# Kernel optimization log

Measured on AMD Instinct MI355X. Metric: run time of the kernel, lower is better.

The kernel has to match this reference:

```python
import jax, jax.numpy as jnp
import numpy as np

N_HEAD = 8
EPS_LN = 1e-5
EPS_SM = 1e-16


def _mlp(x, w1, b1, g, beta, w2, b2):
    # Linear -> ReLU -> LayerNorm -> Linear (matches nn.Sequential in torch module)
    h = jax.nn.relu(x @ w1 + b1)
    mu = jnp.mean(h, axis=-1, keepdims=True)
    var = jnp.mean((h - mu) ** 2, axis=-1, keepdims=True)
    h = (h - mu) * jax.lax.rsqrt(var + EPS_LN) * g + beta
    return h @ w2 + b2


def setup_inputs() -> dict:
    B, L, D, E, Fe, H = 4, 4096, 128, 262144, 5, N_HEAD
    ks = jax.random.split(jax.random.key(0), 20)
    s = 0.02
    p = lambda i, sh: jax.random.normal(ks[i], sh, jnp.float32) * s
    z = lambda n: jnp.zeros((n,), jnp.float32)
    inp = {
        "key": jax.random.normal(ks[0], (B, L, D), jnp.float32),
        "value": jax.random.normal(ks[1], (B, L, D), jnp.float32),
        "query": jax.random.normal(ks[2], (B, L, D), jnp.float32),
        "edge_feats": jax.random.normal(ks[3], (E, Fe), jnp.float32),
        "atten_masks": jnp.zeros((E,), jnp.float32),  # present in signature, unused in forward
        "batch_indices": jax.random.randint(ks[4], (E,), 0, B),
        "head_indices": jax.random.randint(ks[5], (E,), 0, L),
        "tail_indices": jax.random.randint(ks[6], (E,), 0, L),
        "key_w": p(7, (D, D)), "key_b": z(D),
        "query_w": p(8, (D, D)), "query_b": z(D),
        "value_w": p(9, (D, D)), "value_b": z(D),
        "proj_w": p(10, (D, D)), "proj_b": z(D),
        "ea_w1": p(11, (Fe, D)), "ea_b1": z(D), "ea_g": jnp.ones((D,), jnp.float32), "ea_beta": z(D), "ea_w2": p(12, (D, H)), "ea_b2": z(H),
        "ek_w1": p(13, (Fe, D)), "ek_b1": z(D), "ek_g": jnp.ones((D,), jnp.float32), "ek_beta": z(D), "ek_w2": p(14, (D, D)), "ek_b2": z(D),
        "ev_w1": p(15, (Fe, D)), "ev_b1": z(D), "ev_g": jnp.ones((D,), jnp.float32), "ev_beta": z(D), "ev_w2": p(16, (D, D)), "ev_b2": z(D),
    }
    return inp


def reference(key, value, query, edge_feats, atten_masks,
              batch_indices, head_indices, tail_indices,
              key_w, key_b, query_w, query_b, value_w, value_b, proj_w, proj_b,
              ea_w1, ea_b1, ea_g, ea_beta, ea_w2, ea_b2,
              ek_w1, ek_b1, ek_g, ek_beta, ek_w2, ek_b2,
              ev_w1, ev_b1, ev_g, ev_beta, ev_w2, ev_b2):
    B, L, D = query.shape
    H = N_HEAD
    dh = D // H
    N = B * L
    # node projections -> [B*L, H, dh]
    k = (key @ key_w + key_b).reshape(N, H, dh)
    q = (query @ query_w + query_b).reshape(N, H, dh)
    v = (value @ value_w + value_b).reshape(N, H, dh)
    heads = batch_indices * L + head_indices  # destination node per edge
    tails = batch_indices * L + tail_indices  # source node per edge
    # per-edge gather + edge-conditioned k/v
    qs = q[heads]
    ks = k[tails] + _mlp(edge_feats, ek_w1, ek_b1, ek_g, ek_beta, ek_w2, ek_b2).reshape(-1, H, dh)
    vs = v[tails] + _mlp(edge_feats, ev_w1, ev_b1, ev_g, ev_beta, ev_w2, ev_b2).reshape(-1, H, dh)
    w = jnp.sum(ks * qs, axis=-1) + _mlp(edge_feats, ea_w1, ea_b1, ea_g, ea_beta, ea_w2, ea_b2)  # [E, H]
    # segment softmax over edges grouped by destination node
    m = jax.ops.segment_max(w, heads, num_segments=N)
    ex = jnp.exp(w - m[heads])
    denom = jax.ops.segment_sum(ex, heads, num_segments=N)
    att = ex / (denom[heads] + EPS_SM)  # [E, H]
    # weighted scatter-sum combine
    y = jax.ops.segment_sum(att[:, :, None] * vs, heads, num_segments=N).reshape(B, L, D)
    return y @ proj_w + proj_b
```

## Files before the change

### kernel.cpp

```cpp
#include <hip/hip_runtime.h>
#include <hip/hip_bf16.h>

#define D      128
#define NHEAD  8
#define FE     5
#define LSEQ   4096
#define EPB    64
#define NNODE  16384
#define EPS_LN 1e-5f
#define EPS_SM 1e-16f

typedef unsigned short ushort_t;
typedef __bf16 bf16x8 __attribute__((ext_vector_type(8)));
typedef float  f32x4  __attribute__((ext_vector_type(4)));

__device__ __forceinline__ ushort_t f2bf(float x) {
    __hip_bfloat16 b = __float2bfloat16(x);
    return __builtin_bit_cast(unsigned short, b);
}
__device__ __forceinline__ float bf2f(ushort_t u) {
    __hip_bfloat16 b = __builtin_bit_cast(__hip_bfloat16, u);
    return __bfloat162float(b);
}

union Pk8 { ushort_t u[8]; uint4 v; };

__global__ __launch_bounds__(256) void setup_kernel(
    const float* __restrict__ key, const float* __restrict__ value,
    const float* __restrict__ query,
    const float* __restrict__ key_w, const float* __restrict__ key_b,
    const float* __restrict__ value_w, const float* __restrict__ value_b,
    const float* __restrict__ query_w, const float* __restrict__ query_b,
    ushort_t* __restrict__ k16, ushort_t* __restrict__ v16, ushort_t* __restrict__ q16,
    const float* __restrict__ ekw2, const float* __restrict__ evw2,
    const float* __restrict__ eaw2,
    ushort_t* __restrict__ eksw, ushort_t* __restrict__ evsw, ushort_t* __restrict__ easw,
    const int* __restrict__ bidx, const int* __restrict__ hidx,
    int* __restrict__ cnt, int nqb, int E)
{
    __shared__ float xs[2][D][20];
    const int t  = threadIdx.x;
    const int nq = 3 * nqb;

    if ((int)blockIdx.x < nq) {
        const int which = blockIdx.x / nqb;
        const int r0    = (blockIdx.x % nqb) * 32;
        const float* X = (which == 0) ? key   : (which == 1) ? value   : query;
        const float* W = (which == 0) ? key_w : (which == 1) ? value_w : query_w;
        const float* bias = (which == 0) ? key_b : (which == 1) ? value_b : query_b;
        ushort_t* Y = (which == 0) ? k16 : (which == 1) ? v16 : q16;

        const int rg = t >> 7, j = t & 127;
        const int rbase = r0 + rg * 16;
        {
            float tmp[16];
            #pragma unroll
            for (int r = 0; r < 16; ++r) tmp[r] = X[(size_t)(rbase + r) * D + j];
            #pragma unroll
            for (int c = 0; c < 4; ++c)
                *(float4*)&xs[rg][j][c * 4] = float4{tmp[c*4], tmp[c*4+1], tmp[c*4+2], tmp[c*4+3]};
        }
        __syncthreads();
        float acc[16];
        const float b = bias[j];
        #pragma unroll
        for (int r = 0; r < 16; ++r) acc[r] = b;
        #pragma unroll 4
        for (int i = 0; i < D; ++i) {
            const float w = W[i * D + j];
            #pragma unroll
            for (int c = 0; c < 4; ++c) {
                const float4 x4 = *(const float4*)&xs[rg][i][c * 4];
                acc[c*4+0] = fmaf(x4.x, w, acc[c*4+0]);
                acc[c*4+1] = fmaf(x4.y, w, acc[c*4+1]);
                acc[c*4+2] = fmaf(x4.z, w, acc[c*4+2]);
                acc[c*4+3] = fmaf(x4.w, w, acc[c*4+3]);
            }
        }
        #pragma unroll
        for (int r = 0; r < 16; ++r) Y[(size_t)(rbase + r) * D + j] = f2bf(acc[r]);
        return;
    }

    const int b2 = blockIdx.x - nq;
    if (b2 < 17) {
        const int g = b2 * 256 + t;
        const float* src; ushort_t* dst; int frag, ncols, nvalid;
        if (g < 2048)      { src = ekw2; dst = eksw; frag = g;        ncols = 128; nvalid = 128; }
        else if (g < 4096) { src = evw2; dst = evsw; frag = g - 2048; ncols = 128; nvalid = 128; }
        else if (g < 4352) { src = eaw2; dst = easw; frag = g - 4096; ncols = 8;   nvalid = 8; }
        else return;
        const int s = (frag >> 6) & 3;
        const int l = frag & 63;
        const int n = ((frag >> 8) << 4) + (l & 15);
        Pk8 pk;
        #pragma unroll
        for (int j = 0; j < 8; ++j) {
            const int k = s * 32 + (l >> 4) * 8 + j;
            const float v = (n < nvalid) ? src[k * ncols + n] : 0.f;
            pk.u[j] = f2bf(v);
        }
        *(uint4*)(dst + (size_t)frag * 8) = pk.v;
        return;
    }

    const int e = (b2 - 17) * 256 + t;
    if (e < E) atomicAdd(&cnt[bidx[e] * LSEQ + hidx[e]], 1);
}

__global__ __launch_bounds__(1024) void scan16k(
    const int* __restrict__ cnt, int* __restrict__ base)
{
    __shared__ int part[1024];
    const int t = threadIdx.x;
    int v[16], ex[16], s = 0;
    #pragma unroll
    for (int i = 0; i < 16; ++i) v[i] = cnt[t * 16 + i];
    #pragma unroll
    for (int i = 0; i < 16; ++i) { ex[i] = s; s += v[i]; }
    part[t] = s;
    __syncthreads();
    for (int off = 1; off < 1024; off <<= 1) {
        const int x = (t >= off) ? part[t - off] : 0;
        __syncthreads();
        part[t] += x;
        __syncthreads();
    }
    const int boff = (t > 0) ? part[t - 1] : 0;
    #pragma unroll
    for (int i = 0; i < 16; ++i) base[t * 16 + i] = boff + ex[i];
    if (t == 1023) base[NNODE] = boff + s;
}

__global__ __launch_bounds__(128) void out_gemm(
    const float* __restrict__ num, const float* __restrict__ W,
    const float* __restrict__ bias, float* __restrict__ Y)
{
    __shared__ float xs[D][20];
    const int j  = threadIdx.x;
    const int r0 = blockIdx.x * 16;
    {
        float tmp[16];
        #pragma unroll
        for (int r = 0; r < 16; ++r) tmp[r] = num[(size_t)(r0 + r) * D + j];
        #pragma unroll
        for (int c = 0; c < 4; ++c)
            *(float4*)&xs[j][c * 4] = float4{tmp[c*4], tmp[c*4+1], tmp[c*4+2], tmp[c*4+3]};
    }
    __syncthreads();
    float acc[16];
    const float b = bias[j];
    #pragma unroll
    for (int r = 0; r < 16; ++r) acc[r] = b;
    #pragma unroll 4
    for (int i = 0; i < D; ++i) {
        const float w = W[i * D + j];
        #pragma unroll
        for (int c = 0; c < 4; ++c) {
            const float4 x4 = *(const float4*)&xs[i][c * 4];
            acc[c*4+0] = fmaf(x4.x, w, acc[c*4+0]);
            acc[c*4+1] = fmaf(x4.y, w, acc[c*4+1]);
            acc[c*4+2] = fmaf(x4.z, w, acc[c*4+2]);
            acc[c*4+3] = fmaf(x4.w, w, acc[c*4+3]);
        }
    }
    #pragma unroll
    for (int r = 0; r < 16; ++r) Y[(size_t)(r0 + r) * D + j] = acc[r];
}

__global__ __launch_bounds__(256, 4) void edge_kernel(
    const float* __restrict__ edge_feats,
    const int* __restrict__ bidx, const int* __restrict__ hidx, const int* __restrict__ tidx,
    const float* __restrict__ ea_w1, const float* __restrict__ ea_b1,
    const float* __restrict__ ea_g,  const float* __restrict__ ea_be, const float* __restrict__ ea_b2,
    const float* __restrict__ ek_w1, const float* __restrict__ ek_b1,
    const float* __restrict__ ek_g,  const float* __restrict__ ek_be, const float* __restrict__ ek_b2,
    const float* __restrict__ ev_w1, const float* __restrict__ ev_b1,
    const float* __restrict__ ev_g,  const float* __restrict__ ev_be, const float* __restrict__ ev_b2,
    const ushort_t* __restrict__ easw, const ushort_t* __restrict__ eksw, const ushort_t* __restrict__ evsw,
    const ushort_t* __restrict__ k16, const ushort_t* __restrict__ q16, const ushort_t* __restrict__ v16,
    const int* __restrict__ base, int* __restrict__ cnt, int* __restrict__ order,
    float* __restrict__ ex_ws, ushort_t* __restrict__ vs_ws)
{
    __shared__ float pw1[3][FE * D];
    __shared__ float pb1[3][D], pg[3][D], pbe[3][D];
    __shared__ float pb2k[D], pb2v[D], pb2a[NHEAD];
    __shared__ float ef_s[EPB][FE];
    __shared__ int   eh_s[EPB], et_s[EPB];

    const int t   = threadIdx.x;
    const int e0g = blockIdx.x * EPB;

    for (int i = t; i < FE * D; i += 256) { pw1[0][i] = ea_w1[i]; pw1[1][i] = ek_w1[i]; pw1[2][i] = ev_w1[i]; }
    if (t < D) {
        pb1[0][t] = ea_b1[t]; pb1[1][t] = ek_b1[t]; pb1[2][t] = ev_b1[t];
        pg [0][t] = ea_g [t]; pg [1][t] = ek_g [t]; pg [2][t] = ev_g [t];
        pbe[0][t] = ea_be[t]; pbe[1][t] = ek_be[t]; pbe[2][t] = ev_be[t];
        pb2k[t] = ek_b2[t];   pb2v[t] = ev_b2[t];
        if (t < NHEAD) pb2a[t] = ea_b2[t];
    }
    for (int i = t; i < EPB * FE; i += 256) ((float*)ef_s)[i] = edge_feats[(size_t)e0g * FE + i];
    if (t < EPB) {
        const int bb = bidx[e0g + t];
        const int nh = bb * LSEQ + hidx[e0g + t];
        eh_s[t] = nh;
        et_s[t] = bb * LSEQ + tidx[e0g + t];
        const int slot = atomicSub(&cnt[nh], 1) - 1;
        order[base[nh] + slot] = e0g + t;
    }
    __syncthreads();

    const int mt   = t >> 6;
    const int l    = t & 63;
    const int qt   = l & 3;
    const int per  = l >> 2;
    const int row0 = (l >> 4) * 4;
    const int colb = l & 15;
    const int src  = 4 * colb + (l >> 4);
    const int bsrc = (l & 48);

    int tn[4], hnn[4];
    #pragma unroll
    for (int r = 0; r < 4; ++r) { tn[r] = et_s[mt*16 + row0 + r]; hnn[r] = eh_s[mt*16 + row0 + r]; }

    float efr[FE];
    #pragma unroll
    for (int f = 0; f < FE; ++f) efr[f] = ef_s[mt*16 + per][f];

    auto first_layer = [&](int m, uint4 pk[4]) {
        const float4* w1v = (const float4*)&pw1[m][0];
        const float4* b1v = (const float4*)&pb1[m][0];
        const float4* gv  = (const float4*)&pg[m][0];
        const float4* bev = (const float4*)&pbe[m][0];
        float4 hv[4][2];
        float s1 = 0.f, s2 = 0.f;
        #pragma unroll
        for (int s = 0; s < 4; ++s) {
            #pragma unroll
            for (int hc = 0; hc < 2; ++hc) {
                const int idx = s * 8 + qt * 2 + hc;
                float4 a = b1v[idx];
                #pragma unroll
                for (int f = 0; f < FE; ++f) {
                    const float sc = efr[f];
                    const float4 w = w1v[f * 32 + idx];
                    a.x = fmaf(sc, w.x, a.x); a.y = fmaf(sc, w.y, a.y);
                    a.z = fmaf(sc, w.z, a.z); a.w = fmaf(sc, w.w, a.w);
                }
                a.x = fmaxf(a.x, 0.f); a.y = fmaxf(a.y, 0.f);
                a.z = fmaxf(a.z, 0.f); a.w = fmaxf(a.w, 0.f);
                hv[s][hc] = a;
                s1 += a.x + a.y + a.z + a.w;
                s2 += a.x*a.x + a.y*a.y + a.z*a.z + a.w*a.w;
            }
        }
        s1 += __shfl_xor(s1, 1); s1 += __shfl_xor(s1, 2);
        s2 += __shfl_xor(s2, 1); s2 += __shfl_xor(s2, 2);
        const float mu = s1 * (1.f / 128.f);
        const float rs = rsqrtf(s2 * (1.f / 128.f) - mu * mu + EPS_LN);
        #pragma unroll
        for (int s = 0; s < 4; ++s) {
            const int idx = s * 8 + qt * 2;
            const float4 x0 = hv[s][0], x1 = hv[s][1];
            const float4 g0 = gv[idx], g1 = gv[idx + 1];
            const float4 b0 = bev[idx], b1 = bev[idx + 1];
            Pk8 p8;
            p8.u[0] = f2bf(fmaf((x0.x - mu) * rs, g0.x, b0.x));
            p8.u[1] = f2bf(fmaf((x0.y - mu) * rs, g0.y, b0.y));
            p8.u[2] = f2bf(fmaf((x0.z - mu) * rs, g0.z, b0.z));
            p8.u[3] = f2bf(fmaf((x0.w - mu) * rs, g0.w, b0.w));
            p8.u[4] = f2bf(fmaf((x1.x - mu) * rs, g1.x, b1.x));
            p8.u[5] = f2bf(fmaf((x1.y - mu) * rs, g1.y, b1.y));
            p8.u[6] = f2bf(fmaf((x1.z - mu) * rs, g1.z, b1.z));
            p8.u[7] = f2bf(fmaf((x1.w - mu) * rs, g1.w, b1.w));
            pk[s] = p8.v;
        }
    };

    auto gather_afr = [&](const uint4 pk[4], bf16x8 afr[4]) {
        #pragma unroll
        for (int s = 0; s < 4; ++s) {
            uint4 w;
            w.x = (unsigned)__shfl((int)pk[s].x, src);
            w.y = (unsigned)__shfl((int)pk[s].y, src);
            w.z = (unsigned)__shfl((int)pk[s].z, src);
            w.w = (unsigned)__shfl((int)pk[s].w, src);
            afr[s] = __builtin_bit_cast(bf16x8, w);
        }
    };

    uint4 pk[4];
    bf16x8 afr[4];

    float eaacc[4];
    first_layer(0, pk);
    gather_afr(pk, afr);
    {
        f32x4 acc = {0.f, 0.f, 0.f, 0.f};
        #pragma unroll
        for (int s = 0; s < 4; ++s) {
            const bf16x8 bfr = *(const bf16x8*)(easw + (size_t)(s * 64 + l) * 8);
            acc = __builtin_amdgcn_mfma_f32_16x16x32_bf16(afr[s], bfr, acc, 0, 0, 0);
        }
        #pragma unroll
        for (int r = 0; r < 4; ++r) eaacc[r] = acc[r];
    }

    first_layer(1, pk);
    gather_afr(pk, afr);
    #pragma unroll
    for (int nt = 0; nt < NHEAD; ++nt) {
        f32x4 acc = {0.f, 0.f, 0.f, 0.f};
        #pragma unroll
        for (int s = 0; s < 4; ++s) {
            const bf16x8 bfr = *(const bf16x8*)(eksw + (size_t)((nt * 4 + s) * 64 + l) * 8);
            acc = __builtin_amdgcn_mfma_f32_16x16x32_bf16(afr[s], bfr, acc, 0, 0, 0);
        }
        const int col = nt * 16 + colb;
        const float b2 = pb2k[col];
        const float ba = pb2a[nt];
        float pr[4];
        #pragma unroll
        for (int r = 0; r < 4; ++r)
            pr[r] = (acc[r] + b2 + bf2f(k16[(size_t)tn[r] * D + col]))
                    * bf2f(q16[(size_t)hnn[r] * D + col]);
        #pragma unroll
        for (int m = 1; m < 16; m <<= 1) {
            #pragma unroll
            for (int r = 0; r < 4; ++r) pr[r] += __shfl_xor(pr[r], m);
        }
        #pragma unroll
        for (int r = 0; r < 4; ++r) {
            const float ea = __shfl(eaacc[r], bsrc | nt);
            const float ex = __expf(pr[r] + ea + ba);
            if (colb == nt)
                ex_ws[(size_t)(e0g + mt*16 + row0 + r) * NHEAD + nt] = ex;
        }
    }

    first_layer(2, pk);
    gather_afr(pk, afr);
    #pragma unroll
    for (int nt = 0; nt < NHEAD; ++nt) {
        f32x4 acc = {0.f, 0.f, 0.f, 0.f};
        #pragma unroll
        for (int s = 0; s < 4; ++s) {
            const bf16x8 bfr = *(const bf16x8*)(evsw + (size_t)((nt * 4 + s) * 64 + l) * 8);
            acc = __builtin_amdgcn_mfma_f32_16x16x32_bf16(afr[s], bfr, acc, 0, 0, 0);
        }
        const int col = nt * 16 + colb;
        const float b2 = pb2v[col];
        #pragma unroll
        for (int r = 0; r < 4; ++r) {
            const float vs = acc[r] + b2 + bf2f(v16[(size_t)tn[r] * D + col]);
            vs_ws[(size_t)(e0g + mt*16 + row0 + r) * D + col] = f2bf(vs);
        }
    }
}

__global__ __launch_bounds__(128) void agg_kernel(
    const int* __restrict__ order, const int* __restrict__ base,
    const float* __restrict__ ex_ws, const ushort_t* __restrict__ vs_ws,
    float* __restrict__ y_ws)
{
    const int n  = blockIdx.x;
    const int j  = threadIdx.x;
    const int h  = j >> 4;
    const int s0 = base[n], s1 = base[n + 1];

    float acc = 0.f, den = 0.f;
    int i = s0;
    for (; i + 8 <= s1; i += 8) {
        int e[8];
        #pragma unroll
        for (int r = 0; r < 8; ++r) e[r] = order[i + r];
        float exv[8], vsv[8];
        #pragma unroll
        for (int r = 0; r < 8; ++r) {
            exv[r] = ex_ws[(size_t)e[r] * NHEAD + h];
            vsv[r] = bf2f(vs_ws[(size_t)e[r] * D + j]);
        }
        #pragma unroll
        for (int r = 0; r < 8; ++r) {
            den += exv[r];
            acc = fmaf(exv[r], vsv[r], acc);
        }
    }
    for (; i < s1; ++i) {
        const int e = order[i];
        const float ex = ex_ws[(size_t)e * NHEAD + h];
        den += ex;
        acc = fmaf(ex, bf2f(vs_ws[(size_t)e * D + j]), acc);
    }
    y_ws[(size_t)n * D + j] = acc / (den + EPS_SM);
}

extern "C" void kernel_launch(void* const* d_in, const int* in_sizes, int n_in,
                              void* d_out, int out_size, void* d_ws, size_t ws_size,
                              hipStream_t stream)
{
    const float* key        = (const float*)d_in[0];
    const float* value      = (const float*)d_in[1];
    const float* query      = (const float*)d_in[2];
    const float* edge_feats = (const float*)d_in[3];
    const int*   bidx       = (const int*)d_in[5];
    const int*   hidx       = (const int*)d_in[6];
    const int*   tidx       = (const int*)d_in[7];
    const float* key_w   = (const float*)d_in[8];  const float* key_b   = (const float*)d_in[9];
    const float* query_w = (const float*)d_in[10]; const float* query_b = (const float*)d_in[11];
    const float* value_w = (const float*)d_in[12]; const float* value_b = (const float*)d_in[13];
    const float* proj_w  = (const float*)d_in[14]; const float* proj_b  = (const float*)d_in[15];

    const int N = in_sizes[0] / D;
    const int E = in_sizes[5];

    char* ws = (char*)d_ws;
    ushort_t* k16   = (ushort_t*)ws; ws += (size_t)N * D * 2;
    ushort_t* q16   = (ushort_t*)ws; ws += (size_t)N * D * 2;
    ushort_t* v16   = (ushort_t*)ws; ws += (size_t)N * D * 2;
    float* y_ws     = (float*)ws;    ws += (size_t)N * D * 4;
    float* ex_ws    = (float*)ws;    ws += (size_t)E * NHEAD * 4;
    ushort_t* vs_ws = (ushort_t*)ws; ws += (size_t)E * D * 2;
    ushort_t* eksw  = (ushort_t*)ws; ws += (size_t)2048 * 8 * 2;
    ushort_t* evsw  = (ushort_t*)ws; ws += (size_t)2048 * 8 * 2;
    ushort_t* easw  = (ushort_t*)ws; ws += (size_t)256 * 8 * 2;
    int* order = (int*)ws;  ws += (size_t)E * 4;
    int* base  = (int*)ws;  ws += (size_t)(N + 1) * 4;
    int* cnt   = (int*)ws;  ws += (size_t)N * 4;

    const int nqb = N / 32;
    const int nhist = (E + 255) / 256;
    const int ngrid = 3 * nqb + 17 + nhist;

    hipMemsetAsync(cnt, 0, (size_t)N * 4, stream);

    setup_kernel<<<ngrid, 256, 0, stream>>>(
        key, value, query,
        key_w, key_b, value_w, value_b, query_w, query_b,
        k16, v16, q16,
        (const float*)d_in[26], (const float*)d_in[32], (const float*)d_in[20],
        eksw, evsw, easw,
        bidx, hidx, cnt, nqb, E);

    scan16k<<<1, 1024, 0, stream>>>(cnt, base);

    edge_kernel<<<E / EPB, 256, 0, stream>>>(
        edge_feats, bidx, hidx, tidx,
        (const float*)d_in[16], (const float*)d_in[17], (const float*)d_in[18],
        (const float*)d_in[19], (const float*)d_in[21],
        (const float*)d_in[22], (const float*)d_in[23], (const float*)d_in[24],
        (const float*)d_in[25], (const float*)d_in[27],
        (const float*)d_in[28], (const float*)d_in[29], (const float*)d_in[30],
        (const float*)d_in[31], (const float*)d_in[33],
        easw, eksw, evsw,
        k16, q16, v16,
        base, cnt, order,
        ex_ws, vs_ws);

    agg_kernel<<<N, 128, 0, stream>>>(order, base, ex_ws, vs_ws, y_ws);

    out_gemm<<<N / 16, 128, 0, stream>>>(y_ws, proj_w, proj_b, (float*)d_out);
}
```

Measured before the change: 321.9 us.

## Sort edges by destination before edge kernel, fuse scan and output projection

```diff
diff --git a/kernel.cpp b/kernel.cpp
--- a/kernel.cpp
+++ b/kernel.cpp
@@ -22,6 +22,8 @@
     __hip_bfloat16 b = __builtin_bit_cast(__hip_bfloat16, u);
     return __bfloat162float(b);
 }
+__device__ __forceinline__ float i2f(int x)  { return __builtin_bit_cast(float, x); }
+__device__ __forceinline__ int   f2i(float x){ return __builtin_bit_cast(int, x); }
 
 union Pk8 { ushort_t u[8]; uint4 v; };
 
@@ -36,13 +38,14 @@
     const float* __restrict__ eaw2,
     ushort_t* __restrict__ eksw, ushort_t* __restrict__ evsw, ushort_t* __restrict__ easw,
     const int* __restrict__ bidx, const int* __restrict__ hidx,
-    int* __restrict__ cnt, int nqb, int E)
+    int* __restrict__ cnt, int* __restrict__ done, int* __restrict__ base,
+    int nqb, int nhist, int E)
 {
-    __shared__ float xs[2][D][20];
     const int t  = threadIdx.x;
     const int nq = 3 * nqb;
 
     if ((int)blockIdx.x < nq) {
+        __shared__ float xs[2][D][20];
         const int which = blockIdx.x / nqb;
         const int r0    = (blockIdx.x % nqb) * 32;
         const float* X = (which == 0) ? key   : (which == 1) ? value   : query;
@@ -104,73 +107,65 @@
         return;
     }
 
-    const int e = (b2 - 17) * 256 + t;
-    if (e < E) atomicAdd(&cnt[bidx[e] * LSEQ + hidx[e]], 1);
-}
-
-__global__ __launch_bounds__(1024) void scan16k(
-    const int* __restrict__ cnt, int* __restrict__ base)
-{
-    __shared__ int part[1024];
-    const int t = threadIdx.x;
-    int v[16], ex[16], s = 0;
-    #pragma unroll
-    for (int i = 0; i < 16; ++i) v[i] = cnt[t * 16 + i];
-    #pragma unroll
-    for (int i = 0; i < 16; ++i) { ex[i] = s; s += v[i]; }
-    part[t] = s;
+    {
+        const int e = (b2 - 17) * 256 + t;
+        if (e < E) atomicAdd(&cnt[bidx[e] * LSEQ + hidx[e]], 1);
+    }
     __syncthreads();
-    for (int off = 1; off < 1024; off <<= 1) {
+    __threadfence();
+    __shared__ int amLast;
+    if (t == 0) {
+        const int d = __hip_atomic_fetch_add(done, 1, __ATOMIC_ACQ_REL,
+                                             __HIP_MEMORY_SCOPE_AGENT);
+        amLast = (d == nhist - 1);
+    }
+    __syncthreads();
+    if (!amLast) return;
+
+    __shared__ int part[256];
+    int sum = 0;
+    for (int i = 0; i < 64; ++i)
+        sum += __hip_atomic_load(&cnt[t * 64 + i], __ATOMIC_RELAXED,
+                                 __HIP_MEMORY_SCOPE_AGENT);
+    part[t] = sum;
+    __syncthreads();
+    for (int off = 1; off < 256; off <<= 1) {
         const int x = (t >= off) ? part[t - off] : 0;
         __syncthreads();
         part[t] += x;
         __syncthreads();
     }
-    const int boff = (t > 0) ? part[t - 1] : 0;
-    #pragma unroll
-    for (int i = 0; i < 16; ++i) base[t * 16 + i] = boff + ex[i];
-    if (t == 1023) base[NNODE] = boff + s;
-}
-
-__global__ __launch_bounds__(128) void out_gemm(
-    const float* __restrict__ num, const float* __restrict__ W,
-    const float* __restrict__ bias, float* __restrict__ Y)
+    int run = (t > 0) ? part[t - 1] : 0;
+    for (int i = 0; i < 64; ++i) {
+        base[t * 64 + i] = run;
+        run += __hip_atomic_load(&cnt[t * 64 + i], __ATOMIC_RELAXED,
+                                 __HIP_MEMORY_SCOPE_AGENT);
+    }
+    if (t == 255) base[NNODE] = run;
+}
+
+__global__ __launch_bounds__(256) void scatter_rec(
+    const int* __restrict__ bidx, const int* __restrict__ hidx, const int* __restrict__ tidx,
+    const float* __restrict__ edge_feats,
+    const int* __restrict__ base, int* __restrict__ cnt,
+    float* __restrict__ rec, int E)
 {
-    __shared__ float xs[D][20];
-    const int j  = threadIdx.x;
-    const int r0 = blockIdx.x * 16;
-    {
-        float tmp[16];
-        #pragma unroll
-        for (int r = 0; r < 16; ++r) tmp[r] = num[(size_t)(r0 + r) * D + j];
-        #pragma unroll
-        for (int c = 0; c < 4; ++c)
-            *(float4*)&xs[j][c * 4] = float4{tmp[c*4], tmp[c*4+1], tmp[c*4+2], tmp[c*4+3]};
-    }
-    __syncthreads();
-    float acc[16];
-    const float b = bias[j];
-    #pragma unroll
-    for (int r = 0; r < 16; ++r) acc[r] = b;
-    #pragma unroll 4
-    for (int i = 0; i < D; ++i) {
-        const float w = W[i * D + j];
-        #pragma unroll
-        for (int c = 0; c < 4; ++c) {
-            const float4 x4 = *(const float4*)&xs[i][c * 4];
-            acc[c*4+0] = fmaf(x4.x, w, acc[c*4+0]);
-            acc[c*4+1] = fmaf(x4.y, w, acc[c*4+1]);
-            acc[c*4+2] = fmaf(x4.z, w, acc[c*4+2]);
-            acc[c*4+3] = fmaf(x4.w, w, acc[c*4+3]);
-        }
-    }
-    #pragma unroll
-    for (int r = 0; r < 16; ++r) Y[(size_t)(r0 + r) * D + j] = acc[r];
+    const int e = blockIdx.x * 256 + threadIdx.x;
+    if (e >= E) return;
+    const int bb = bidx[e];
+    const int nh = bb * LSEQ + hidx[e];
+    const int nt = bb * LSEQ + tidx[e];
+    const int slot = atomicSub(&cnt[nh], 1) - 1;
+    const int p = base[nh] + slot;
+    float ef[FE];
+    #pragma unroll
+    for (int f = 0; f < FE; ++f) ef[f] = edge_feats[(size_t)e * FE + f];
+    *(float4*)&rec[(size_t)p * 8]     = float4{ef[0], ef[1], ef[2], ef[3]};
+    *(float4*)&rec[(size_t)p * 8 + 4] = float4{ef[4], i2f(nh), i2f(nt), 0.f};
 }
 
 __global__ __launch_bounds__(256, 4) void edge_kernel(
-    const float* __restrict__ edge_feats,
-    const int* __restrict__ bidx, const int* __restrict__ hidx, const int* __restrict__ tidx,
+    const float* __restrict__ rec,
     const float* __restrict__ ea_w1, const float* __restrict__ ea_b1,
     const float* __restrict__ ea_g,  const float* __restrict__ ea_be, const float* __restrict__ ea_b2,
     const float* __restrict__ ek_w1, const float* __restrict__ ek_b1,
@@ -179,7 +174,6 @@
     const float* __restrict__ ev_g,  const float* __restrict__ ev_be, const float* __restrict__ ev_b2,
     const ushort_t* __restrict__ easw, const ushort_t* __restrict__ eksw, const ushort_t* __restrict__ evsw,
     const ushort_t* __restrict__ k16, const ushort_t* __restrict__ q16, const ushort_t* __restrict__ v16,
-    const int* __restrict__ base, int* __restrict__ cnt, int* __restrict__ order,
     float* __restrict__ ex_ws, ushort_t* __restrict__ vs_ws)
 {
     __shared__ float pw1[3][FE * D];
@@ -199,14 +193,14 @@
         pb2k[t] = ek_b2[t];   pb2v[t] = ev_b2[t];
         if (t < NHEAD) pb2a[t] = ea_b2[t];
     }
-    for (int i = t; i < EPB * FE; i += 256) ((float*)ef_s)[i] = edge_feats[(size_t)e0g * FE + i];
-    if (t < EPB) {
-        const int bb = bidx[e0g + t];
-        const int nh = bb * LSEQ + hidx[e0g + t];
-        eh_s[t] = nh;
-        et_s[t] = bb * LSEQ + tidx[e0g + t];
-        const int slot = atomicSub(&cnt[nh], 1) - 1;
-        order[base[nh] + slot] = e0g + t;
+    if (t < 128) {
+        const int pl = t >> 1, half = t & 1;
+        const float4 v = *(const float4*)&rec[((size_t)e0g + pl) * 8 + half * 4];
+        if (half == 0) {
+            ef_s[pl][0] = v.x; ef_s[pl][1] = v.y; ef_s[pl][2] = v.z; ef_s[pl][3] = v.w;
+        } else {
+            ef_s[pl][4] = v.x; eh_s[pl] = f2i(v.y); et_s[pl] = f2i(v.z);
+        }
     }
     __syncthreads();
 
@@ -358,41 +352,63 @@
     }
 }
 
-__global__ __launch_bounds__(128) void agg_kernel(
-    const int* __restrict__ order, const int* __restrict__ base,
+__global__ __launch_bounds__(256) void agg_out(
+    const int* __restrict__ base,
     const float* __restrict__ ex_ws, const ushort_t* __restrict__ vs_ws,
-    float* __restrict__ y_ws)
+    const float* __restrict__ W, const float* __restrict__ bias,
+    float* __restrict__ out)
 {
-    const int n  = blockIdx.x;
-    const int j  = threadIdx.x;
+    __shared__ float xs[D][20];
+    const int t  = threadIdx.x;
+    const int rg = t >> 7;
+    const int j  = t & 127;
     const int h  = j >> 4;
-    const int s0 = base[n], s1 = base[n + 1];
-
-    float acc = 0.f, den = 0.f;
-    int i = s0;
-    for (; i + 8 <= s1; i += 8) {
-        int e[8];
-        #pragma unroll
-        for (int r = 0; r < 8; ++r) e[r] = order[i + r];
-        float exv[8], vsv[8];
-        #pragma unroll
-        for (int r = 0; r < 8; ++r) {
-            exv[r] = ex_ws[(size_t)e[r] * NHEAD + h];
-            vsv[r] = bf2f(vs_ws[(size_t)e[r] * D + j]);
-        }
-        #pragma unroll
-        for (int r = 0; r < 8; ++r) {
-            den += exv[r];
-            acc = fmaf(exv[r], vsv[r], acc);
-        }
-    }
-    for (; i < s1; ++i) {
-        const int e = order[i];
-        const float ex = ex_ws[(size_t)e * NHEAD + h];
-        den += ex;
-        acc = fmaf(ex, bf2f(vs_ws[(size_t)e * D + j]), acc);
-    }
-    y_ws[(size_t)n * D + j] = acc / (den + EPS_SM);
+    const int n0 = blockIdx.x * 16;
+
+    for (int ni = 0; ni < 8; ++ni) {
+        const int n  = n0 + rg * 8 + ni;
+        const int s0 = base[n], s1 = base[n + 1];
+        float acc = 0.f, den = 0.f;
+        int p = s0;
+        for (; p + 4 <= s1; p += 4) {
+            float ex4[4], vs4[4];
+            #pragma unroll
+            for (int r = 0; r < 4; ++r) {
+                ex4[r] = ex_ws[(size_t)(p + r) * NHEAD + h];
+                vs4[r] = bf2f(vs_ws[(size_t)(p + r) * D + j]);
+            }
+            #pragma unroll
+            for (int r = 0; r < 4; ++r) {
+                den += ex4[r];
+                acc = fmaf(ex4[r], vs4[r], acc);
+            }
+        }
+        for (; p < s1; ++p) {
+            const float ex = ex_ws[(size_t)p * NHEAD + h];
+            den += ex;
+            acc = fmaf(ex, bf2f(vs_ws[(size_t)p * D + j]), acc);
+        }
+        xs[j][rg * 8 + ni] = acc / (den + EPS_SM);
+    }
+    __syncthreads();
+
+    float acc[8];
+    const float b = bias[j];
+    #pragma unroll
+    for (int r = 0; r < 8; ++r) acc[r] = b;
+    #pragma unroll 4
+    for (int i = 0; i < D; ++i) {
+        const float w = W[i * D + j];
+        const float4 y0 = *(const float4*)&xs[i][rg * 8];
+        const float4 y1 = *(const float4*)&xs[i][rg * 8 + 4];
+        acc[0] = fmaf(y0.x, w, acc[0]); acc[1] = fmaf(y0.y, w, acc[1]);
+        acc[2] = fmaf(y0.z, w, acc[2]); acc[3] = fmaf(y0.w, w, acc[3]);
+        acc[4] = fmaf(y1.x, w, acc[4]); acc[5] = fmaf(y1.y, w, acc[5]);
+        acc[6] = fmaf(y1.z, w, acc[6]); acc[7] = fmaf(y1.w, w, acc[7]);
+    }
+    #pragma unroll
+    for (int r = 0; r < 8; ++r)
+        out[(size_t)(n0 + rg * 8 + r) * D + j] = acc[r];
 }
 
 extern "C" void kernel_launch(void* const* d_in, const int* in_sizes, int n_in,
@@ -418,21 +434,21 @@
     ushort_t* k16   = (ushort_t*)ws; ws += (size_t)N * D * 2;
     ushort_t* q16   = (ushort_t*)ws; ws += (size_t)N * D * 2;
     ushort_t* v16   = (ushort_t*)ws; ws += (size_t)N * D * 2;
-    float* y_ws     = (float*)ws;    ws += (size_t)N * D * 4;
     float* ex_ws    = (float*)ws;    ws += (size_t)E * NHEAD * 4;
     ushort_t* vs_ws = (ushort_t*)ws; ws += (size_t)E * D * 2;
+    float* rec      = (float*)ws;    ws += (size_t)E * 8 * 4;
     ushort_t* eksw  = (ushort_t*)ws; ws += (size_t)2048 * 8 * 2;
     ushort_t* evsw  = (ushort_t*)ws; ws += (size_t)2048 * 8 * 2;
     ushort_t* easw  = (ushort_t*)ws; ws += (size_t)256 * 8 * 2;
-    int* order = (int*)ws;  ws += (size_t)E * 4;
-    int* base  = (int*)ws;  ws += (size_t)(N + 1) * 4;
-    int* cnt   = (int*)ws;  ws += (size_t)N * 4;
-
-    const int nqb = N / 32;
+    int* base = (int*)ws;  ws += (size_t)(N + 1) * 4;
+    int* cnt  = (int*)ws;  ws += (size_t)N * 4;
+    int* done = (int*)ws;  ws += 4;
+
+    const int nqb   = N / 32;
     const int nhist = (E + 255) / 256;
     const int ngrid = 3 * nqb + 17 + nhist;
 
-    hipMemsetAsync(cnt, 0, (size_t)N * 4, stream);
+    hipMemsetAsync(cnt, 0, (size_t)(N + 1) * 4, stream);
 
     setup_kernel<<<ngrid, 256, 0, stream>>>(
         key, value, query,
@@ -440,12 +456,13 @@
         k16, v16, q16,
         (const float*)d_in[26], (const float*)d_in[32], (const float*)d_in[20],
         eksw, evsw, easw,
-        bidx, hidx, cnt, nqb, E);
-
-    scan16k<<<1, 1024, 0, stream>>>(cnt, base);
+        bidx, hidx, cnt, done, base, nqb, nhist, E);
+
+    scatter_rec<<<(E + 255) / 256, 256, 0, stream>>>(
+        bidx, hidx, tidx, edge_feats, base, cnt, rec, E);
 
     edge_kernel<<<E / EPB, 256, 0, stream>>>(
-        edge_feats, bidx, hidx, tidx,
+        rec,
         (const float*)d_in[16], (const float*)d_in[17], (const float*)d_in[18],
         (const float*)d_in[19], (const float*)d_in[21],
         (const float*)d_in[22], (const float*)d_in[23], (const float*)d_in[24],
@@ -454,10 +471,7 @@
         (const float*)d_in[31], (const float*)d_in[33],
         easw, eksw, evsw,
         k16, q16, v16,
-        base, cnt, order,
         ex_ws, vs_ws);
 
-    agg_kernel<<<N, 128, 0, stream>>>(order, base, ex_ws, vs_ws, y_ws);
-
-    out_gemm<<<N / 16, 128, 0, stream>>>(y_ws, proj_w, proj_b, (float*)d_out);
-}
+    agg_out<<<N / 16, 256, 0, stream>>>(base, ex_ws, vs_ws, proj_w, proj_b, (float*)d_out);
+}
```

Result: slower. 427.2 us (+32.7%).
